# Optimization experiments

Hardware: AMD Instinct MI355X
Metric: run time of the kernel (lower is better)

The kernel has to match this reference:

```python
import jax, jax.numpy as jnp
import numpy as np

B, S, E, H = 8, 1024, 1024, 16
D = E // H  # head_dim = 64
NEG_INF = jnp.finfo(jnp.float32).min


def setup_inputs() -> dict:
    key = jax.random.key(0)
    ks = jax.random.split(key, 14)
    w = 0.02  # init scale for projection weights
    inp = {
        "query": jax.random.normal(ks[0], (B, S, E), jnp.float32),
        "key": jax.random.normal(ks[1], (B, S, E), jnp.float32),
        "value": jax.random.normal(ks[2], (B, S, E), jnp.float32),
        "attn_bias": jax.random.normal(ks[3], (B, H, S, S), jnp.float32),
        "key_padding_mask": jax.random.randint(ks[4], (B, S), 0, 2).astype(bool),
        "attn_mask": jnp.zeros((S, S), jnp.float32),
        "need_weights": 0,
        "before_softmax": 0,
        "need_head_weights": 0,
        "Wq": jax.random.normal(ks[5], (E, E), jnp.float32) * w,
        "bq": jnp.zeros((E,), jnp.float32),
        "Wk": jax.random.normal(ks[6], (E, E), jnp.float32) * w,
        "bk": jnp.zeros((E,), jnp.float32),
        "Wv": jax.random.normal(ks[7], (E, E), jnp.float32) * w,
        "bv": jnp.zeros((E,), jnp.float32),
        "Wo": jax.random.normal(ks[8], (E, E), jnp.float32) * w,
        "bo": jnp.zeros((E,), jnp.float32),
    }
    return inp


def reference(query, key, value, attn_bias, key_padding_mask, attn_mask,
              need_weights, before_softmax, need_head_weights,
              Wq, bq, Wk, bk, Wv, bv, Wo, bo):
    # self_attention=True: torch code projects q, k, v ALL from `query`.
    scaling = D ** -0.5
    q = (query @ Wq.T + bq) * scaling          # [B,S,E]
    k = query @ Wk.T + bk
    v = query @ Wv.T + bv
    q = q.reshape(B, S, H, D)
    k = k.reshape(B, S, H, D)
    v = v.reshape(B, S, H, D)
    # scores: QK^T + bias + mask, materialized [B,H,S,S] like the torch bmm
    scores = jnp.einsum('bqhd,bkhd->bhqk', q, k)
    scores = scores + attn_bias
    scores = scores + attn_mask[None, None]    # attn_mask broadcast over B,H
    scores = jnp.where(key_padding_mask[:, None, None, :], NEG_INF, scores)
    probs = jax.nn.softmax(scores, axis=-1)    # dropout p=0.0 -> identity
    attn = jnp.einsum('bhqk,bkhd->bqhd', probs, v).reshape(B, S, E)
    out = attn @ Wo.T + bo                     # [B,S,E]
    # need_weights=False path: torch returns (attn, None); return attn only.
    return out
```

## Files before the change

kernel.cpp:

```cpp
#include <hip/hip_runtime.h>

#define B_ 8
#define S_ 1024
#define E_ 1024
#define H_ 16
#define D_ 64

typedef __attribute__((ext_vector_type(8))) short bf16x8;
typedef __attribute__((ext_vector_type(4))) float floatx4;

__device__ __forceinline__ floatx4 mfma16x16x32(bf16x8 a, bf16x8 b, floatx4 c) {
  return __builtin_amdgcn_mfma_f32_16x16x32_bf16(a, b, c, 0, 0, 0);
}

__device__ __forceinline__ unsigned short f2bf(float x) {
  unsigned int u = __builtin_bit_cast(unsigned int, x);
  u += 0x7FFFu + ((u >> 16) & 1u);
  return (unsigned short)(u >> 16);
}

__device__ __forceinline__ void async16(const unsigned short* g, unsigned short* l) {
  __builtin_amdgcn_global_load_lds(
      (const __attribute__((address_space(1))) void*)g,
      (__attribute__((address_space(3))) void*)l, 16, 0, 0);
}

__global__ void mask_prep(const unsigned int* __restrict__ mraw, float* __restrict__ maskadd) {
  __shared__ int flagF, flagB;
  const int tid = threadIdx.x;
  if (tid == 0) { flagF = 0; flagB = 0; }
  __syncthreads();
  int lf = 0, lb = 0;
  for (int i = tid; i < 2048; i += 256) {
    unsigned int v = mraw[i];
    if (v == 0x3F800000u) lf = 1;
    else if (v > 1u) lb = 1;
  }
  if (lf) atomicOr(&flagF, 1);
  if (lb) atomicOr(&flagB, 1);
  __syncthreads();
  const unsigned char* mb = (const unsigned char*)mraw;
  const float* mf = (const float*)mraw;
  const int* mi = (const int*)mraw;
  const int fF = flagF, fB = flagB;
  for (int i = tid; i < B_ * S_; i += 256) {
    int pad;
    if (fF)      pad = (mf[i] != 0.0f);
    else if (fB) pad = (mb[i] != 0);
    else         pad = (mi[i] != 0);
    maskadd[i] = pad ? -3.4028234663852886e38f : 0.0f;
  }
}

__global__ __launch_bounds__(256) void convert_prep(
    const float* __restrict__ q, const float* __restrict__ wq, const float* __restrict__ wk,
    const float* __restrict__ wv, const float* __restrict__ wo,
    unsigned short* __restrict__ xb, unsigned short* __restrict__ wqb,
    unsigned short* __restrict__ wkb, unsigned short* __restrict__ wvb,
    unsigned short* __restrict__ wob)
{
  size_t idx = (size_t)blockIdx.x * 256 + threadIdx.x;
  const float* src; unsigned short* dst; size_t off;
  if (idx < 2097152)      { src = q;  dst = xb;  off = idx; }
  else if (idx < 2359296) { src = wq; dst = wqb; off = idx - 2097152; }
  else if (idx < 2621440) { src = wk; dst = wkb; off = idx - 2359296; }
  else if (idx < 2883584) { src = wv; dst = wvb; off = idx - 2621440; }
  else                    { src = wo; dst = wob; off = idx - 2883584; }
  float4 v = *(const float4*)(src + off * 4);
  ushort4 u; u.x = f2bf(v.x); u.y = f2bf(v.y); u.z = f2bf(v.z); u.w = f2bf(v.w);
  *(ushort4*)(dst + off * 4) = u;
}

__device__ __forceinline__ void gemm_core(
    const unsigned short* __restrict__ A, const unsigned short* __restrict__ Bm,
    int m0, int n0, unsigned short* As, unsigned short* Bs, floatx4 (&acc)[4][4])
{
  const int tid = threadIdx.x;
  const int wave = tid >> 6, lane = tid & 63;
  const int quad = lane >> 4, l16 = lane & 15;
  const int mb = (wave >> 1) * 64, nb = (wave & 1) * 64;
  const int ldrow = lane >> 3;
  const int gchunk = (lane & 7) ^ ldrow;

  for (int ks = 0; ks < 16; ++ks) {
    const int k0 = ks * 64;
    __syncthreads();
    for (int is = 0; is < 4; ++is) {
      int issue = wave * 4 + is;
      async16(A + (size_t)(m0 + issue * 8 + ldrow) * 1024 + k0 + gchunk * 8, &As[issue * 512]);
      async16(Bm + (size_t)(n0 + issue * 8 + ldrow) * 1024 + k0 + gchunk * 8, &Bs[issue * 512]);
    }
    __syncthreads();
    for (int kk = 0; kk < 2; ++kk) {
      const int pc = ((quad + 4 * kk) ^ (l16 & 7)) * 8;
      bf16x8 af[4], bfm[4];
      for (int i = 0; i < 4; ++i)
        af[i] = *(const bf16x8*)(&As[(mb + 16 * i + l16) * 64 + pc]);
      for (int j = 0; j < 4; ++j)
        bfm[j] = *(const bf16x8*)(&Bs[(nb + 16 * j + l16) * 64 + pc]);
      for (int i = 0; i < 4; ++i)
        for (int j = 0; j < 4; ++j)
          acc[i][j] = mfma16x16x32(af[i], bfm[j], acc[i][j]);
    }
  }
}

__global__ __launch_bounds__(256) void gemm_qkv(
    const unsigned short* __restrict__ Xbf,
    const unsigned short* __restrict__ Wqb, const unsigned short* __restrict__ Wkb,
    const unsigned short* __restrict__ Wvb,
    const float* __restrict__ bq, const float* __restrict__ bk, const float* __restrict__ bv,
    unsigned short* __restrict__ qo, unsigned short* __restrict__ ko, unsigned short* __restrict__ vo)
{
  const int tid = threadIdx.x;
  const int flat = blockIdx.y * 24 + blockIdx.x;
  const int swz = (flat & 7) * 192 + (flat >> 3);
  const int bx = swz % 24, by = swz / 24;
  const int n0 = bx * 128;
  const int m0 = by * 128;
  const int which = n0 >> 10;
  const int nn0 = n0 & 1023;
  const unsigned short* W = (which == 0) ? Wqb : (which == 1) ? Wkb : Wvb;
  const float* bias = (which == 0) ? bq : (which == 1) ? bk : bv;

  __shared__ unsigned short smem[128 * 136];
  unsigned short* As = smem;
  unsigned short* Bs = smem + 8192;

  const int lane = tid & 63, wave = tid >> 6;
  const int quad = lane >> 4, l16 = lane & 15;
  const int mb = (wave >> 1) * 64, nb = (wave & 1) * 64;

  floatx4 z = {0.f, 0.f, 0.f, 0.f};
  floatx4 acc[4][4];
  for (int i = 0; i < 4; ++i) for (int j = 0; j < 4; ++j) acc[i][j] = z;

  gemm_core(Xbf, W, m0, nn0, As, Bs, acc);

  float bv4[4];
  for (int j = 0; j < 4; ++j) bv4[j] = bias[nn0 + nb + 16 * j + l16];

  __syncthreads();

  const float scale = (which == 0) ? 0.125f : 1.0f;
  if (which < 2) {
    #pragma unroll
    for (int i = 0; i < 4; ++i)
      #pragma unroll
      for (int r = 0; r < 4; ++r) {
        const int mr = mb + 16 * i + quad * 4 + r;
        #pragma unroll
        for (int j = 0; j < 4; ++j)
          smem[mr * 136 + nb + 16 * j + l16] = f2bf((acc[i][j][r] + bv4[j]) * scale);
      }
  } else {
    #pragma unroll
    for (int i = 0; i < 4; ++i)
      #pragma unroll
      for (int r = 0; r < 4; ++r) {
        const int mr = mb + 16 * i + quad * 4 + r;
        #pragma unroll
        for (int j = 0; j < 4; ++j)
          smem[(nb + 16 * j + l16) * 136 + mr] = f2bf(acc[i][j][r] + bv4[j]);
      }
  }
  __syncthreads();

  const int row = tid >> 1, half = tid & 1;
  if (which < 2) {
    const int m = m0 + row, bb = m >> 10, s = m & 1023;
    const int hh = (nn0 >> 6) + half;
    unsigned short* dst = ((which == 0) ? qo : ko) +
        ((size_t)(bb * 16 + hh) * 1024 + s) * 64;
    #pragma unroll
    for (int c = 0; c < 8; ++c)
      *(bf16x8*)(dst + c * 8) = *(const bf16x8*)(&smem[row * 136 + half * 64 + c * 8]);
  } else {
    const int nglob = nn0 + row;
    const int hh = nglob >> 6, d = nglob & 63;
    const int bb = m0 >> 10;
    unsigned short* dst = vo + ((size_t)(bb * 16 + hh) * 64 + d) * 1024 +
        (m0 & 1023) + half * 64;
    #pragma unroll
    for (int c = 0; c < 8; ++c)
      *(bf16x8*)(dst + c * 8) = *(const bf16x8*)(&smem[row * 136 + half * 64 + c * 8]);
  }
}

__global__ __launch_bounds__(256) void gemm_out(
    const unsigned short* __restrict__ Abf, const unsigned short* __restrict__ Wob,
    const float* __restrict__ bo, float* __restrict__ out)
{
  const int flat = blockIdx.y * 8 + blockIdx.x;
  const int swz = (flat & 7) * 64 + (flat >> 3);
  const int n0 = (swz & 7) * 128;
  const int m0 = (swz >> 3) * 128;
  __shared__ unsigned short As[128 * 64];
  __shared__ unsigned short Bs[128 * 64];

  const int lane = threadIdx.x & 63, wave = threadIdx.x >> 6;
  const int quad = lane >> 4, l16 = lane & 15;
  const int mb = (wave >> 1) * 64, nb = (wave & 1) * 64;

  floatx4 z = {0.f, 0.f, 0.f, 0.f};
  floatx4 acc[4][4];
  for (int i = 0; i < 4; ++i) for (int j = 0; j < 4; ++j) acc[i][j] = z;

  gemm_core(Abf, Wob, m0, n0, As, Bs, acc);

  for (int i = 0; i < 4; ++i) {
    for (int r = 0; r < 4; ++r) {
      int m = m0 + mb + 16 * i + quad * 4 + r;
      for (int j = 0; j < 4; ++j) {
        int n = n0 + nb + 16 * j + l16;
        out[(size_t)m * 1024 + n] = acc[i][j][r] + bo[n];
      }
    }
  }
}

__global__ __launch_bounds__(256) void attn_fwd(
    const unsigned short* __restrict__ qw, const unsigned short* __restrict__ kw,
    const unsigned short* __restrict__ vw, const float* __restrict__ bias,
    const float* __restrict__ amask, const float* __restrict__ maskadd,
    unsigned short* __restrict__ attnw)
{
  const int tid = threadIdx.x;
  const int wave = tid >> 6, lane = tid & 63;
  const int quad = lane >> 4, l16 = lane & 15;
  const int flat = blockIdx.y * 16 + blockIdx.x;
  const int swz = (flat & 7) * 256 + (flat >> 3);
  const int qt = swz & 15, bh = swz >> 4;
  const int b = bh >> 4, h = bh & 15;
  const int qbase = qt * 64 + wave * 16;

  const unsigned short* qh = qw + (size_t)bh * (S_ * D_);
  const unsigned short* kh = kw + (size_t)bh * (S_ * D_);
  const unsigned short* vh = vw + (size_t)bh * (S_ * D_);
  const float* biasb = bias + (size_t)bh * ((size_t)S_ * S_) +
                       (size_t)(qt * 64 + wave * 16 + quad * 4) * S_;
  const float* amrow = amask + (size_t)(qt * 64 + wave * 16 + quad * 4) * S_;
  const float* madd  = maskadd + b * S_;

  __shared__ unsigned short Vt[64 * 64];
  __shared__ unsigned short P_lds[4 * 16 * 72];
  unsigned short* Pw = &P_lds[wave * (16 * 72)];

  const int vrow = tid >> 3;
  const int vchk = tid & 7;

  bf16x8 aQ0 = *(const bf16x8*)(qh + (size_t)(qbase + l16) * 64 + quad * 8);
  bf16x8 aQ1 = *(const bf16x8*)(qh + (size_t)(qbase + l16) * 64 + 32 + quad * 8);

  bf16x8 pv[2];
  float cc[4][4], nc[4][4];

  auto load_v = [&](int key0) {
    #pragma unroll
    for (int i2 = 0; i2 < 2; ++i2) {
      int d = vrow + 32 * i2;
      int gc = vchk ^ (d & 7);
      pv[i2] = *(const bf16x8*)(vh + (size_t)d * 1024 + key0 + gc * 8);
    }
  };
  auto load_cinit = [&](int key0, float (&dst)[4][4]) {
    #pragma unroll
    for (int t = 0; t < 4; ++t) {
      const int col = key0 + 16 * t + l16;
      const float mv = madd[col];
      #pragma unroll
      for (int r = 0; r < 4; ++r)
        dst[t][r] = biasb[(size_t)r * S_ + col] + amrow[(size_t)r * S_ + col] + mv;
    }
  };
  load_v(0);
  load_cinit(0, cc);

  floatx4 zz = {0.f, 0.f, 0.f, 0.f};
  floatx4 oacc[4] = {zz, zz, zz, zz};
  float m_run[4], l_run[4];
  for (int r = 0; r < 4; ++r) { m_run[r] = -__builtin_inff(); l_run[r] = 0.f; }

  for (int kt = 0; kt < 16; ++kt) {
    const int key0 = kt * 64;
    __syncthreads();
    #pragma unroll
    for (int i2 = 0; i2 < 2; ++i2)
      *(bf16x8*)(&Vt[(vrow + 32 * i2) * 64 + vchk * 8]) = pv[i2];

    bf16x8 bK0[4], bK1[4];
    #pragma unroll
    for (int t = 0; t < 4; ++t) {
      const unsigned short* kr = kh + (size_t)(key0 + 16 * t + l16) * 64;
      bK0[t] = *(const bf16x8*)(kr + quad * 8);
      bK1[t] = *(const bf16x8*)(kr + 32 + quad * 8);
    }
    if (kt < 15) { load_v(key0 + 64); load_cinit(key0 + 64, nc); }
    __syncthreads();

    floatx4 sfr[4];
    #pragma unroll
    for (int t = 0; t < 4; ++t) {
      floatx4 c;
      #pragma unroll
      for (int r = 0; r < 4; ++r) c[r] = cc[t][r];
      c = mfma16x16x32(aQ0, bK0[t], c);
      c = mfma16x16x32(aQ1, bK1[t], c);
      sfr[t] = c;
    }
    #pragma unroll
    for (int r = 0; r < 4; ++r) {
      float rm = fmaxf(fmaxf(sfr[0][r], sfr[1][r]), fmaxf(sfr[2][r], sfr[3][r]));
      rm = fmaxf(rm, __shfl_xor(rm, 1));
      rm = fmaxf(rm, __shfl_xor(rm, 2));
      rm = fmaxf(rm, __shfl_xor(rm, 4));
      rm = fmaxf(rm, __shfl_xor(rm, 8));
      float mnew = fmaxf(m_run[r], rm);
      float alpha = __expf(m_run[r] - mnew);
      float psum = 0.f;
      #pragma unroll
      for (int t = 0; t < 4; ++t) {
        float p = __expf(sfr[t][r] - mnew);
        psum += p;
        Pw[(quad * 4 + r) * 72 + 16 * t + l16] = f2bf(p);
      }
      psum += __shfl_xor(psum, 1);
      psum += __shfl_xor(psum, 2);
      psum += __shfl_xor(psum, 4);
      psum += __shfl_xor(psum, 8);
      l_run[r] = l_run[r] * alpha + psum;
      m_run[r] = mnew;
      oacc[0][r] *= alpha; oacc[1][r] *= alpha; oacc[2][r] *= alpha; oacc[3][r] *= alpha;
    }
    #pragma unroll
    for (int kc = 0; kc < 2; ++kc) {
      bf16x8 aP = *(const bf16x8*)(Pw + l16 * 72 + kc * 32 + quad * 8);
      const int pc = ((kc * 4 + quad) ^ (l16 & 7)) * 8;
      #pragma unroll
      for (int t = 0; t < 4; ++t) {
        bf16x8 bV = *(const bf16x8*)(&Vt[(16 * t + l16) * 64 + pc]);
        oacc[t] = mfma16x16x32(aP, bV, oacc[t]);
      }
    }
    if (kt < 15) {
      #pragma unroll
      for (int t = 0; t < 4; ++t)
        #pragma unroll
        for (int r = 0; r < 4; ++r) cc[t][r] = nc[t][r];
    }
  }

  for (int r = 0; r < 4; ++r) {
    int row = qbase + quad * 4 + r;
    float inv = 1.0f / l_run[r];
    unsigned short* orow = attnw + (size_t)(b * S_ + row) * E_ + h * 64;
    for (int t = 0; t < 4; ++t)
      orow[16 * t + l16] = f2bf(oacc[t][r] * inv);
  }
}

extern "C" void kernel_launch(void* const* d_in, const int* in_sizes, int n_in,
                              void* d_out, int out_size, void* d_ws, size_t ws_size,
                              hipStream_t stream) {
  const float* query      = (const float*)d_in[0];
  const float* attn_bias  = (const float*)d_in[3];
  const unsigned int* kpm = (const unsigned int*)d_in[4];
  const float* amask      = (const float*)d_in[5];
  const float* Wq = (const float*)d_in[9];
  const float* bq = (const float*)d_in[10];
  const float* Wk = (const float*)d_in[11];
  const float* bk = (const float*)d_in[12];
  const float* Wv = (const float*)d_in[13];
  const float* bv = (const float*)d_in[14];
  const float* Wo = (const float*)d_in[15];
  const float* bo = (const float*)d_in[16];

  char* ws = (char*)d_ws;
  const size_t MB16 = 16777216;
  unsigned short* qw    = (unsigned short*)(ws);
  unsigned short* kw    = (unsigned short*)(ws + MB16);
  unsigned short* vw    = (unsigned short*)(ws + 2 * MB16);
  unsigned short* xbf   = (unsigned short*)(ws + 3 * MB16);
  unsigned short* attnw = (unsigned short*)(ws + 3 * MB16);
  unsigned short* wqb   = (unsigned short*)(ws + 4 * MB16);
  unsigned short* wkb   = (unsigned short*)(ws + 4 * MB16 + 2097152);
  unsigned short* wvb   = (unsigned short*)(ws + 4 * MB16 + 2 * 2097152);
  unsigned short* wob   = (unsigned short*)(ws + 4 * MB16 + 3 * 2097152);
  float* maskadd        = (float*)(ws + 4 * MB16 + 4 * 2097152);

  mask_prep<<<1, 256, 0, stream>>>(kpm, maskadd);
  convert_prep<<<12288, 256, 0, stream>>>(query, Wq, Wk, Wv, Wo, xbf, wqb, wkb, wvb, wob);
  gemm_qkv<<<dim3(24, 64), 256, 0, stream>>>(xbf, wqb, wkb, wvb, bq, bk, bv, qw, kw, vw);
  attn_fwd<<<dim3(16, 128), 256, 0, stream>>>(qw, kw, vw, attn_bias, amask, maskadd, attnw);
  gemm_out<<<dim3(8, 64), 256, 0, stream>>>(attnw, wob, bo, (float*)d_out);
}
```

Baseline: 984.8 us.

## Give each wave a private V tile and double-buffer K/bias loads without block barriers

Each wave now loads and transposes its own full 64x64 V tile into a private LDS region, which removes both __syncthreads per key tile. K fragments and bias/mask inits are prefetched two tiles ahead through A/B register sets, alternated by unrolling the loop in pairs. The aim is to drop the block-wide barriers and hide global-load latency. In exchange it adds 4x redundant V loads per block (each wave fetches the whole tile), 4x V LDS usage, and much higher register pressure, which may lower occupancy.

```diff
diff --git a/kernel.cpp b/kernel.cpp
--- a/kernel.cpp
+++ b/kernel.cpp
@@ -238,29 +238,33 @@
   const unsigned short* kh = kw + (size_t)bh * (S_ * D_);
   const unsigned short* vh = vw + (size_t)bh * (S_ * D_);
   const float* biasb = bias + (size_t)bh * ((size_t)S_ * S_) +
-                       (size_t)(qt * 64 + wave * 16 + quad * 4) * S_;
-  const float* amrow = amask + (size_t)(qt * 64 + wave * 16 + quad * 4) * S_;
+                       (size_t)(qbase + quad * 4) * S_;
+  const float* amrow = amask + (size_t)(qbase + quad * 4) * S_;
   const float* madd  = maskadd + b * S_;
 
-  __shared__ unsigned short Vt[64 * 64];
-  __shared__ unsigned short P_lds[4 * 16 * 72];
-  unsigned short* Pw = &P_lds[wave * (16 * 72)];
-
-  const int vrow = tid >> 3;
-  const int vchk = tid & 7;
+  __shared__ unsigned short Vt_all[4][64 * 64];
+  __shared__ unsigned short P_all[4][16 * 72];
+  unsigned short* Vt = Vt_all[wave];
+  unsigned short* Pw = P_all[wave];
+
+  const int srow = lane >> 3;
+  const int schk = lane & 7;
 
   bf16x8 aQ0 = *(const bf16x8*)(qh + (size_t)(qbase + l16) * 64 + quad * 8);
   bf16x8 aQ1 = *(const bf16x8*)(qh + (size_t)(qbase + l16) * 64 + 32 + quad * 8);
 
-  bf16x8 pv[2];
-  float cc[4][4], nc[4][4];
+  bf16x8 pv[8];
 
   auto load_v = [&](int key0) {
     #pragma unroll
-    for (int i2 = 0; i2 < 2; ++i2) {
-      int d = vrow + 32 * i2;
-      int gc = vchk ^ (d & 7);
-      pv[i2] = *(const bf16x8*)(vh + (size_t)d * 1024 + key0 + gc * 8);
+    for (int i = 0; i < 8; ++i)
+      pv[i] = *(const bf16x8*)(vh + (size_t)(srow + 8 * i) * 1024 + key0 + schk * 8);
+  };
+  auto store_v = [&]() {
+    #pragma unroll
+    for (int i = 0; i < 8; ++i) {
+      const int d = srow + 8 * i;
+      *(bf16x8*)(&Vt[d * 64 + ((schk ^ (d & 7)) * 8)]) = pv[i];
     }
   };
   auto load_cinit = [&](int key0, float (&dst)[4][4]) {
@@ -273,39 +277,36 @@
         dst[t][r] = biasb[(size_t)r * S_ + col] + amrow[(size_t)r * S_ + col] + mv;
     }
   };
-  load_v(0);
-  load_cinit(0, cc);
+  auto load_k = [&](int key0, bf16x8 (&K0)[4], bf16x8 (&K1)[4]) {
+    #pragma unroll
+    for (int t = 0; t < 4; ++t) {
+      const unsigned short* kr = kh + (size_t)(key0 + 16 * t + l16) * 64;
+      K0[t] = *(const bf16x8*)(kr + quad * 8);
+      K1[t] = *(const bf16x8*)(kr + 32 + quad * 8);
+    }
+  };
+
+  float ccA[4][4], ccB[4][4];
+  bf16x8 kA0[4], kA1[4], kB0[4], kB1[4];
+
+  load_v(0); load_cinit(0, ccA); load_k(0, kA0, kA1);
+  store_v();
+  load_v(64); load_cinit(64, ccB); load_k(64, kB0, kB1);
 
   floatx4 zz = {0.f, 0.f, 0.f, 0.f};
   floatx4 oacc[4] = {zz, zz, zz, zz};
   float m_run[4], l_run[4];
   for (int r = 0; r < 4; ++r) { m_run[r] = -__builtin_inff(); l_run[r] = 0.f; }
 
-  for (int kt = 0; kt < 16; ++kt) {
-    const int key0 = kt * 64;
-    __syncthreads();
-    #pragma unroll
-    for (int i2 = 0; i2 < 2; ++i2)
-      *(bf16x8*)(&Vt[(vrow + 32 * i2) * 64 + vchk * 8]) = pv[i2];
-
-    bf16x8 bK0[4], bK1[4];
-    #pragma unroll
-    for (int t = 0; t < 4; ++t) {
-      const unsigned short* kr = kh + (size_t)(key0 + 16 * t + l16) * 64;
-      bK0[t] = *(const bf16x8*)(kr + quad * 8);
-      bK1[t] = *(const bf16x8*)(kr + 32 + quad * 8);
-    }
-    if (kt < 15) { load_v(key0 + 64); load_cinit(key0 + 64, nc); }
-    __syncthreads();
-
+  auto tile_body = [&](int kt, float (&ci)[4][4], bf16x8 (&K0)[4], bf16x8 (&K1)[4]) {
     floatx4 sfr[4];
     #pragma unroll
     for (int t = 0; t < 4; ++t) {
       floatx4 c;
       #pragma unroll
-      for (int r = 0; r < 4; ++r) c[r] = cc[t][r];
-      c = mfma16x16x32(aQ0, bK0[t], c);
-      c = mfma16x16x32(aQ1, bK1[t], c);
+      for (int r = 0; r < 4; ++r) c[r] = ci[t][r];
+      c = mfma16x16x32(aQ0, K0[t], c);
+      c = mfma16x16x32(aQ1, K1[t], c);
       sfr[t] = c;
     }
     #pragma unroll
@@ -342,12 +343,17 @@
         oacc[t] = mfma16x16x32(aP, bV, oacc[t]);
       }
     }
-    if (kt < 15) {
-      #pragma unroll
-      for (int t = 0; t < 4; ++t)
-        #pragma unroll
-        for (int r = 0; r < 4; ++r) cc[t][r] = nc[t][r];
-    }
+    if (kt < 15) store_v();
+    if (kt < 14) {
+      load_v((kt + 2) * 64);
+      load_cinit((kt + 2) * 64, ci);
+      load_k((kt + 2) * 64, K0, K1);
+    }
+  };
+
+  for (int k2 = 0; k2 < 8; ++k2) {
+    tile_body(2 * k2,     ccA, kA0, kA1);
+    tile_body(2 * k2 + 1, ccB, kB0, kB1);
   }
 
   for (int r = 0; r < 4; ++r) {
```

New measurement: 1.086 ms. +10.3%, slower.
